# Kernel tuning notes

Hardware: AMD Instinct MI355X
Metric: run time of the kernel (lower is better)

Reference implementation:

```python
import jax, jax.numpy as jnp
import numpy as np

B, S, H, D = 2, 2048, 16, 128  # batch, seq, n_head, head_dim; n_embd = H*D
N_EMBD = H * D

def setup_inputs() -> dict:
    key = jax.random.key(0)
    kq, kk, kv = jax.random.split(key, 3)
    q = jax.random.normal(kq, (B, S, H, D), dtype=jnp.float32)
    k = jax.random.normal(kk, (B, S, H, D), dtype=jnp.float32)
    v = jax.random.normal(kv, (B, S, H, D), dtype=jnp.float32)
    return {"q": q, "k": k, "v": v}

def reference(q, k, v):
    # [B,S,H,D] -> [B,H,S,D]
    qh = jnp.transpose(q, (0, 2, 1, 3))
    kh = jnp.transpose(k, (0, 2, 1, 3))
    vh = jnp.transpose(v, (0, 2, 1, 3))
    # scores scaled by head_dim (NOT sqrt), matching the original module
    att = jnp.einsum('bhqd,bhkd->bhqk', qh, kh) / D
    att = jax.nn.softmax(att, axis=-1)
    y = jnp.einsum('bhqk,bhkd->bhqd', att, vh)
    # [B,H,S,D] -> [B,S,H,D] -> [B*S, n_embd]
    y = jnp.transpose(y, (0, 2, 1, 3)).reshape(B * S, N_EMBD)
    return y
```

## Files before the change

### kernel.cpp

```cpp
#include <hip/hip_runtime.h>


#define SEQ   2048
#define NHEAD 16
#define DH    128
#define NB    2
#define BQ    128
#define BK    64
#define NTHR  256
#define KSTR  136
#define VSTR  72
#define PSTR  40
#define NKV   (SEQ / BK)
#define NELEM (NB * SEQ * NHEAD * DH)

typedef __attribute__((ext_vector_type(8)))  short bf16x8;
typedef __attribute__((ext_vector_type(16))) float f32x16;

__device__ __forceinline__ unsigned short f2bf(float x) {
    unsigned int u = __builtin_bit_cast(unsigned int, x);
    u += 0x7fffu + ((u >> 16) & 1u);
    return (unsigned short)(u >> 16);
}

__global__ __launch_bounds__(256) void cvt_bf16(
    const float* __restrict__ q, const float* __restrict__ k,
    const float* __restrict__ v, unsigned short* __restrict__ dst)
{
    const int y = blockIdx.y;
    const float* s = (y == 0) ? q : (y == 1) ? k : v;
    unsigned short* d = dst + (size_t)y * NELEM;
    const int i = blockIdx.x * 256 + threadIdx.x;
    const float4 x = ((const float4*)s)[i];
    ushort4 o;
    o.x = f2bf(x.x); o.y = f2bf(x.y); o.z = f2bf(x.z); o.w = f2bf(x.w);
    ((ushort4*)d)[i] = o;
}

__global__ __launch_bounds__(NTHR, 2) void attn_fwd(
    const unsigned short* __restrict__ Qb,
    const unsigned short* __restrict__ Kb,
    const unsigned short* __restrict__ Vb,
    float* __restrict__ O)
{
    __shared__ unsigned short Kl[2][BK * KSTR];
    __shared__ unsigned short Vl[2][DH * VSTR];
    __shared__ unsigned short Pt[BQ * PSTR];

    const int tid  = threadIdx.x;
    const int wave = tid >> 6;
    const int lane = tid & 63;
    const int hx   = lane >> 5;
    const int l32  = lane & 31;

    const int b  = blockIdx.y >> 4;
    const int h  = blockIdx.y & 15;
    const int q0 = blockIdx.x * BQ;

    const size_t rs = (size_t)NHEAD * DH;
    const unsigned short* qb = Qb + (size_t)b * SEQ * rs + (size_t)h * DH;
    const unsigned short* kb = Kb + (size_t)b * SEQ * rs + (size_t)h * DH;
    const unsigned short* vb = Vb + (size_t)b * SEQ * rs + (size_t)h * DH;

    bf16x8 qf[8];
    {
        const unsigned short* qp = qb + (size_t)(q0 + wave * 32 + l32) * rs + hx * 8;
        #pragma unroll
        for (int c = 0; c < 8; ++c)
            qf[c] = *(const bf16x8*)(qp + c * 16);
    }

    int kgo[4], kls[4];
    #pragma unroll
    for (int p = 0; p < 4; ++p) {
        const int cidx = (wave * 4 + p) * 64 + lane;
        const int key  = cidx >> 4;
        const int cc   = cidx & 15;
        kgo[p] = key * (int)rs + cc * 8;
        kls[p] = key * KSTR + cc * 8;
    }
    const int kp  = tid & 31;
    const int dcv = tid >> 5;

    f32x16 o4[4];
    #pragma unroll
    for (int t = 0; t < 4; ++t)
        #pragma unroll
        for (int r = 0; r < 16; ++r) o4[t][r] = 0.f;
    float lsum = 0.f;
    const float c1 = 1.44269504088896340736f / 128.0f;

    bf16x8 kr[4], vr[4];

    {
        #pragma unroll
        for (int p = 0; p < 4; ++p) kr[p] = *(const bf16x8*)(kb + kgo[p]);
        #pragma unroll
        for (int p = 0; p < 2; ++p) {
            const unsigned short* src = vb + (size_t)(2 * kp) * rs + (dcv + p * 8) * 8;
            vr[p * 2]     = *(const bf16x8*)src;
            vr[p * 2 + 1] = *(const bf16x8*)(src + rs);
        }
        #pragma unroll
        for (int p = 0; p < 4; ++p) *(bf16x8*)&Kl[0][kls[p]] = kr[p];
        unsigned int* vw = (unsigned int*)&Vl[0][0];
        #pragma unroll
        for (int p = 0; p < 2; ++p)
            #pragma unroll
            for (int j = 0; j < 8; ++j) {
                const unsigned int pr = ((unsigned int)(unsigned short)vr[p * 2][j])
                                      | (((unsigned int)(unsigned short)vr[p * 2 + 1][j]) << 16);
                vw[((dcv + p * 8) * 8 + j) * (VSTR / 2) + kp] = pr;
            }
    }
    __syncthreads();

    const int prow = (wave * 32 + l32) * PSTR;

    for (int kv = 0; kv < NKV; ++kv) {
        const int cur = kv & 1;
        const int k0n = ((kv + 1) & (NKV - 1)) * BK;

        #pragma unroll
        for (int p = 0; p < 4; ++p) kr[p] = *(const bf16x8*)(kb + (size_t)k0n * rs + kgo[p]);
        #pragma unroll
        for (int p = 0; p < 2; ++p) {
            const unsigned short* src = vb + (size_t)(k0n + 2 * kp) * rs + (dcv + p * 8) * 8;
            vr[p * 2]     = *(const bf16x8*)src;
            vr[p * 2 + 1] = *(const bf16x8*)(src + rs);
        }

        const unsigned short* Kc = &Kl[cur][0];
        const unsigned short* Vc = &Vl[cur][0];

        #pragma unroll
        for (int kt = 0; kt < 2; ++kt) {
            f32x16 s;
            #pragma unroll
            for (int r = 0; r < 16; ++r) s[r] = 0.f;
            #pragma unroll
            for (int c = 0; c < 8; ++c) {
                bf16x8 kf = *(const bf16x8*)&Kc[(kt * 32 + l32) * KSTR + c * 16 + hx * 8];
                s = __builtin_amdgcn_mfma_f32_32x32x16_bf16(kf, qf[c], s, 0, 0, 0);
            }
            #pragma unroll
            for (int g = 0; g < 4; ++g) {
                const float e0 = __builtin_amdgcn_exp2f(s[g * 4 + 0] * c1);
                const float e1 = __builtin_amdgcn_exp2f(s[g * 4 + 1] * c1);
                const float e2 = __builtin_amdgcn_exp2f(s[g * 4 + 2] * c1);
                const float e3 = __builtin_amdgcn_exp2f(s[g * 4 + 3] * c1);
                lsum += (e0 + e1) + (e2 + e3);
                ushort4 pk;
                pk.x = (unsigned short)(__builtin_bit_cast(unsigned int, e0) >> 16);
                pk.y = (unsigned short)(__builtin_bit_cast(unsigned int, e1) >> 16);
                pk.z = (unsigned short)(__builtin_bit_cast(unsigned int, e2) >> 16);
                pk.w = (unsigned short)(__builtin_bit_cast(unsigned int, e3) >> 16);
                *(ushort4*)&Pt[prow + g * 8 + hx * 4] = pk;
            }
            #pragma unroll
            for (int ks = 0; ks < 2; ++ks) {
                bf16x8 pf = *(const bf16x8*)&Pt[prow + ks * 16 + hx * 8];
                #pragma unroll
                for (int dt = 0; dt < 4; ++dt) {
                    bf16x8 vf = *(const bf16x8*)&Vc[(dt * 32 + l32) * VSTR
                                                    + kt * 32 + ks * 16 + hx * 8];
                    o4[dt] = __builtin_amdgcn_mfma_f32_32x32x16_bf16(pf, vf, o4[dt], 0, 0, 0);
                }
            }
        }

        const int nxt = cur ^ 1;
        #pragma unroll
        for (int p = 0; p < 4; ++p) *(bf16x8*)&Kl[nxt][kls[p]] = kr[p];
        {
            unsigned int* vw = (unsigned int*)&Vl[nxt][0];
            #pragma unroll
            for (int p = 0; p < 2; ++p)
                #pragma unroll
                for (int j = 0; j < 8; ++j) {
                    const unsigned int pr = ((unsigned int)(unsigned short)vr[p * 2][j])
                                          | (((unsigned int)(unsigned short)vr[p * 2 + 1][j]) << 16);
                    vw[((dcv + p * 8) * 8 + j) * (VSTR / 2) + kp] = pr;
                }
        }
        __syncthreads();
    }

    lsum += __shfl_xor(lsum, 32, 64);
    const float inv = 1.0f / lsum;
    float iv[16];
    #pragma unroll
    for (int r = 0; r < 16; ++r)
        iv[r] = __shfl(inv, (r & 3) + 8 * (r >> 2) + 4 * hx, 64);

    #pragma unroll
    for (int dt = 0; dt < 4; ++dt) {
        #pragma unroll
        for (int r = 0; r < 16; ++r) {
            const int ql = (r & 3) + 8 * (r >> 2) + 4 * hx;
            const int qg = q0 + wave * 32 + ql;
            O[(size_t)(b * SEQ + qg) * rs + (size_t)h * DH + dt * 32 + l32] = o4[dt][r] * iv[r];
        }
    }
}

extern "C" void kernel_launch(void* const* d_in, const int* in_sizes, int n_in,
                              void* d_out, int out_size, void* d_ws, size_t ws_size,
                              hipStream_t stream) {
    const float* q = (const float*)d_in[0];
    const float* k = (const float*)d_in[1];
    const float* v = (const float*)d_in[2];
    float* o = (float*)d_out;
    unsigned short* wsb = (unsigned short*)d_ws;

    cvt_bf16<<<dim3(NELEM / 1024, 3), 256, 0, stream>>>(q, k, v, wsb);
    attn_fwd<<<dim3(SEQ / BQ, NB * NHEAD), dim3(NTHR), 0, stream>>>(
        wsb, wsb + NELEM, wsb + 2 * (size_t)NELEM, o);
}
```

Measured before the change: 215.8 us.

## Double query tile per wave and move P to registers via permlane swap

Each wave now handles 64 query rows (two 32-row tiles), so every K/V fragment read from LDS feeds two MFMAs and the grid has half as many blocks. The P matrix is no longer staged through shared memory; v_permlane32_swap rearranges the packed bf16 exponentials in registers into the layout the PV MFMA expects. The softmax scale is folded into Q during the bf16 conversion. The trade-off is higher register pressure, with occupancy bounds dropped to 1 block/SM, and a grid of only 256 blocks.

```diff
diff --git a/kernel.cpp b/kernel.cpp
--- a/kernel.cpp
+++ b/kernel.cpp
@@ -5,22 +5,31 @@
 #define NHEAD 16
 #define DH    128
 #define NB    2
-#define BQ    128
+#define BQ    256
 #define BK    64
 #define NTHR  256
 #define KSTR  136
 #define VSTR  72
-#define PSTR  40
 #define NKV   (SEQ / BK)
 #define NELEM (NB * SEQ * NHEAD * DH)
 
 typedef __attribute__((ext_vector_type(8)))  short bf16x8;
 typedef __attribute__((ext_vector_type(16))) float f32x16;
+typedef __attribute__((ext_vector_type(4)))  unsigned int u32x4;
 
 __device__ __forceinline__ unsigned short f2bf(float x) {
     unsigned int u = __builtin_bit_cast(unsigned int, x);
     u += 0x7fffu + ((u >> 16) & 1u);
     return (unsigned short)(u >> 16);
+}
+
+__device__ __forceinline__ unsigned int pk2bf(float lo, float hi) {
+    return (__builtin_bit_cast(unsigned int, hi) & 0xffff0000u)
+         | (__builtin_bit_cast(unsigned int, lo) >> 16);
+}
+
+__device__ __forceinline__ void pl32(unsigned int& a, unsigned int& b) {
+    asm("v_permlane32_swap_b32 %0, %1" : "+v"(a), "+v"(b));
 }
 
 __global__ __launch_bounds__(256) void cvt_bf16(
@@ -29,15 +38,17 @@
 {
     const int y = blockIdx.y;
     const float* s = (y == 0) ? q : (y == 1) ? k : v;
+    const float scl = (y == 0) ? (1.44269504088896340736f / 128.0f) : 1.0f;
     unsigned short* d = dst + (size_t)y * NELEM;
     const int i = blockIdx.x * 256 + threadIdx.x;
     const float4 x = ((const float4*)s)[i];
     ushort4 o;
-    o.x = f2bf(x.x); o.y = f2bf(x.y); o.z = f2bf(x.z); o.w = f2bf(x.w);
+    o.x = f2bf(x.x * scl); o.y = f2bf(x.y * scl);
+    o.z = f2bf(x.z * scl); o.w = f2bf(x.w * scl);
     ((ushort4*)d)[i] = o;
 }
 
-__global__ __launch_bounds__(NTHR, 2) void attn_fwd(
+__global__ __launch_bounds__(NTHR, 1) void attn_fwd(
     const unsigned short* __restrict__ Qb,
     const unsigned short* __restrict__ Kb,
     const unsigned short* __restrict__ Vb,
@@ -45,7 +56,6 @@
 {
     __shared__ unsigned short Kl[2][BK * KSTR];
     __shared__ unsigned short Vl[2][DH * VSTR];
-    __shared__ unsigned short Pt[BQ * PSTR];
 
     const int tid  = threadIdx.x;
     const int wave = tid >> 6;
@@ -62,12 +72,14 @@
     const unsigned short* kb = Kb + (size_t)b * SEQ * rs + (size_t)h * DH;
     const unsigned short* vb = Vb + (size_t)b * SEQ * rs + (size_t)h * DH;
 
-    bf16x8 qf[8];
-    {
-        const unsigned short* qp = qb + (size_t)(q0 + wave * 32 + l32) * rs + hx * 8;
+    bf16x8 qf[2][8];
+    #pragma unroll
+    for (int qt = 0; qt < 2; ++qt) {
+        const unsigned short* qp =
+            qb + (size_t)(q0 + wave * 64 + qt * 32 + l32) * rs + hx * 8;
         #pragma unroll
         for (int c = 0; c < 8; ++c)
-            qf[c] = *(const bf16x8*)(qp + c * 16);
+            qf[qt][c] = *(const bf16x8*)(qp + c * 16);
     }
 
     int kgo[4], kls[4];
@@ -82,13 +94,14 @@
     const int kp  = tid & 31;
     const int dcv = tid >> 5;
 
-    f32x16 o4[4];
-    #pragma unroll
-    for (int t = 0; t < 4; ++t)
-        #pragma unroll
-        for (int r = 0; r < 16; ++r) o4[t][r] = 0.f;
-    float lsum = 0.f;
-    const float c1 = 1.44269504088896340736f / 128.0f;
+    f32x16 o4[2][4];
+    #pragma unroll
+    for (int qt = 0; qt < 2; ++qt)
+        #pragma unroll
+        for (int t = 0; t < 4; ++t)
+            #pragma unroll
+            for (int r = 0; r < 16; ++r) o4[qt][t][r] = 0.f;
+    float lsum[2] = {0.f, 0.f};
 
     bf16x8 kr[4], vr[4];
 
@@ -115,8 +128,6 @@
     }
     __syncthreads();
 
-    const int prow = (wave * 32 + l32) * PSTR;
-
     for (int kv = 0; kv < NKV; ++kv) {
         const int cur = kv & 1;
         const int k0n = ((kv + 1) & (NKV - 1)) * BK;
@@ -135,38 +146,59 @@
 
         #pragma unroll
         for (int kt = 0; kt < 2; ++kt) {
-            f32x16 s;
-            #pragma unroll
-            for (int r = 0; r < 16; ++r) s[r] = 0.f;
+            f32x16 s[2];
+            #pragma unroll
+            for (int r = 0; r < 16; ++r) { s[0][r] = 0.f; s[1][r] = 0.f; }
             #pragma unroll
             for (int c = 0; c < 8; ++c) {
                 bf16x8 kf = *(const bf16x8*)&Kc[(kt * 32 + l32) * KSTR + c * 16 + hx * 8];
-                s = __builtin_amdgcn_mfma_f32_32x32x16_bf16(kf, qf[c], s, 0, 0, 0);
+                s[0] = __builtin_amdgcn_mfma_f32_32x32x16_bf16(kf, qf[0][c], s[0], 0, 0, 0);
+                s[1] = __builtin_amdgcn_mfma_f32_32x32x16_bf16(kf, qf[1][c], s[1], 0, 0, 0);
             }
-            #pragma unroll
-            for (int g = 0; g < 4; ++g) {
-                const float e0 = __builtin_amdgcn_exp2f(s[g * 4 + 0] * c1);
-                const float e1 = __builtin_amdgcn_exp2f(s[g * 4 + 1] * c1);
-                const float e2 = __builtin_amdgcn_exp2f(s[g * 4 + 2] * c1);
-                const float e3 = __builtin_amdgcn_exp2f(s[g * 4 + 3] * c1);
-                lsum += (e0 + e1) + (e2 + e3);
-                ushort4 pk;
-                pk.x = (unsigned short)(__builtin_bit_cast(unsigned int, e0) >> 16);
-                pk.y = (unsigned short)(__builtin_bit_cast(unsigned int, e1) >> 16);
-                pk.z = (unsigned short)(__builtin_bit_cast(unsigned int, e2) >> 16);
-                pk.w = (unsigned short)(__builtin_bit_cast(unsigned int, e3) >> 16);
-                *(ushort4*)&Pt[prow + g * 8 + hx * 4] = pk;
-            }
-            #pragma unroll
-            for (int ks = 0; ks < 2; ++ks) {
-                bf16x8 pf = *(const bf16x8*)&Pt[prow + ks * 16 + hx * 8];
+
+            unsigned int w[2][4][2];
+            #pragma unroll
+            for (int qt = 0; qt < 2; ++qt)
+                #pragma unroll
+                for (int g = 0; g < 4; ++g) {
+                    const float e0 = __builtin_amdgcn_exp2f(s[qt][g * 4 + 0]);
+                    const float e1 = __builtin_amdgcn_exp2f(s[qt][g * 4 + 1]);
+                    const float e2 = __builtin_amdgcn_exp2f(s[qt][g * 4 + 2]);
+                    const float e3 = __builtin_amdgcn_exp2f(s[qt][g * 4 + 3]);
+                    lsum[qt] += (e0 + e1) + (e2 + e3);
+                    w[qt][g][0] = pk2bf(e0, e1);
+                    w[qt][g][1] = pk2bf(e2, e3);
+                }
+
+            #pragma unroll
+            for (int qt = 0; qt < 2; ++qt)
+                #pragma unroll
+                for (int ks = 0; ks < 2; ++ks) {
+                    pl32(w[qt][2 * ks][0], w[qt][2 * ks + 1][0]);
+                    pl32(w[qt][2 * ks][1], w[qt][2 * ks + 1][1]);
+                }
+            bf16x8 pf[2][2];
+            #pragma unroll
+            for (int qt = 0; qt < 2; ++qt)
+                #pragma unroll
+                for (int ks = 0; ks < 2; ++ks) {
+                    u32x4 t;
+                    t.x = w[qt][2 * ks][0];
+                    t.y = w[qt][2 * ks][1];
+                    t.z = w[qt][2 * ks + 1][0];
+                    t.w = w[qt][2 * ks + 1][1];
+                    pf[qt][ks] = __builtin_bit_cast(bf16x8, t);
+                }
+
+            #pragma unroll
+            for (int ks = 0; ks < 2; ++ks)
                 #pragma unroll
                 for (int dt = 0; dt < 4; ++dt) {
                     bf16x8 vf = *(const bf16x8*)&Vc[(dt * 32 + l32) * VSTR
                                                     + kt * 32 + ks * 16 + hx * 8];
-                    o4[dt] = __builtin_amdgcn_mfma_f32_32x32x16_bf16(pf, vf, o4[dt], 0, 0, 0);
-                }
-            }
+                    o4[0][dt] = __builtin_amdgcn_mfma_f32_32x32x16_bf16(pf[0][ks], vf, o4[0][dt], 0, 0, 0);
+                    o4[1][dt] = __builtin_amdgcn_mfma_f32_32x32x16_bf16(pf[1][ks], vf, o4[1][dt], 0, 0, 0);
+                }
         }
 
         const int nxt = cur ^ 1;
@@ -186,21 +218,25 @@
         __syncthreads();
     }
 
-    lsum += __shfl_xor(lsum, 32, 64);
-    const float inv = 1.0f / lsum;
-    float iv[16];
-    #pragma unroll
-    for (int r = 0; r < 16; ++r)
-        iv[r] = __shfl(inv, (r & 3) + 8 * (r >> 2) + 4 * hx, 64);
-
-    #pragma unroll
-    for (int dt = 0; dt < 4; ++dt) {
-        #pragma unroll
-        for (int r = 0; r < 16; ++r) {
-            const int ql = (r & 3) + 8 * (r >> 2) + 4 * hx;
-            const int qg = q0 + wave * 32 + ql;
-            O[(size_t)(b * SEQ + qg) * rs + (size_t)h * DH + dt * 32 + l32] = o4[dt][r] * iv[r];
-        }
+    #pragma unroll
+    for (int qt = 0; qt < 2; ++qt) {
+        float ls = lsum[qt];
+        ls += __shfl_xor(ls, 32, 64);
+        const float inv = 1.0f / ls;
+        float iv[16];
+        #pragma unroll
+        for (int r = 0; r < 16; ++r)
+            iv[r] = __shfl(inv, (r & 3) + 8 * (r >> 2) + 4 * hx, 64);
+
+        #pragma unroll
+        for (int dt = 0; dt < 4; ++dt)
+            #pragma unroll
+            for (int r = 0; r < 16; ++r) {
+                const int ql = (r & 3) + 8 * (r >> 2) + 4 * hx;
+                const int qg = q0 + wave * 64 + qt * 32 + ql;
+                O[(size_t)(b * SEQ + qg) * rs + (size_t)h * DH + dt * 32 + l32]
+                    = o4[qt][dt][r] * iv[r];
+            }
     }
 }
 
```

New measurement: 214.5 us. No clear change (-0.6%).
